# Kernel optimization log

Hardware: AMD Instinct MI355X
Metric: run time of the kernel (lower is better)

## Reference

```python
import jax, jax.numpy as jnp
import numpy as np

EMBED_DIM = 1024
NUM_HEADS = 16
HEAD_DIM = EMBED_DIM // NUM_HEADS


def setup_inputs() -> dict:
    key = jax.random.key(0)
    ks = jax.random.split(key, 9)
    B, S, E = 2, 2048, EMBED_DIM
    scale = 1.0 / np.sqrt(E)
    inp = {
        "x": jax.random.normal(ks[0], (B, S, E), dtype=jnp.float32),
        "Wq": jax.random.normal(ks[1], (E, E), dtype=jnp.float32) * scale,
        "bq": jnp.zeros((E,), dtype=jnp.float32),
        "Wk": jax.random.normal(ks[2], (E, E), dtype=jnp.float32) * scale,
        "bk": jnp.zeros((E,), dtype=jnp.float32),
        "Wv": jax.random.normal(ks[3], (E, E), dtype=jnp.float32) * scale,
        "bv": jnp.zeros((E,), dtype=jnp.float32),
        "Wo": jax.random.normal(ks[4], (E, E), dtype=jnp.float32) * scale,
        "bo": jnp.zeros((E,), dtype=jnp.float32),
    }
    return inp


def reference(x, Wq, bq, Wk, bk, Wv, bv, Wo, bo):
    B, S, E = x.shape
    H, D = NUM_HEADS, HEAD_DIM
    sm_scale = D ** (-0.5)

    def proj(W, b):
        # torch Linear: x @ W.T + b ; reshape to [B, H, S, D]
        y = jnp.einsum("bse,fe->bsf", x, W) + b
        return y.reshape(B, S, H, D).transpose(0, 2, 1, 3)

    q = proj(Wq, bq)  # [B, H, S, D]
    k = proj(Wk, bk)
    v = proj(Wv, bv)

    scores = jnp.einsum("bhqd,bhkd->bhqk", q, k) * sm_scale  # [B, H, S, S]
    attn = jax.nn.softmax(scores, axis=-1)
    o = jnp.einsum("bhqk,bhkd->bhqd", attn, v)  # [B, H, S, D]
    o = o.transpose(0, 2, 1, 3).reshape(B, S, E)
    return jnp.einsum("bse,fe->bsf", o, Wo) + bo
```

## Files before the change

kernel.cpp:

```cpp
#include <hip/hip_runtime.h>
#include <hip/hip_fp16.h>
#include <stdint.h>


typedef _Float16 f16;
typedef _Float16 f16x8 __attribute__((ext_vector_type(8)));
typedef _Float16 f16x4v __attribute__((ext_vector_type(4)));
typedef float f32x4 __attribute__((ext_vector_type(4)));
typedef int i32x4 __attribute__((ext_vector_type(4)));

#define BQ  2
#define SEQ 2048
#define EMB 1024
#define NH  16
#define HD  64
#define MM  (BQ * SEQ)

__device__ __forceinline__ void gld_lds16(const void* g, void* l) {
  __builtin_amdgcn_global_load_lds(
      (const __attribute__((address_space(1))) void*)g,
      (__attribute__((address_space(3))) void*)l, 16, 0, 0);
}

__device__ __forceinline__ void stage128x64(const f16* __restrict__ src,
                                            int ld, f16* lds, int tid) {
#pragma unroll
  for (int it = 0; it < 4; ++it) {
    int idx = it * 256 + tid;
    int r = idx >> 3, c = idx & 7;
    int sc = c ^ (r & 7);
    gld_lds16(src + (size_t)r * ld + sc * 8, lds + idx * 8);
  }
}

__device__ __forceinline__ f16x8 pack8(float a0, float a1, float a2, float a3,
                                       float b0, float b1, float b2, float b3) {
  i32x4 w;
  w.x = __builtin_bit_cast(int, __builtin_amdgcn_cvt_pkrtz(a0, a1));
  w.y = __builtin_bit_cast(int, __builtin_amdgcn_cvt_pkrtz(a2, a3));
  w.z = __builtin_bit_cast(int, __builtin_amdgcn_cvt_pkrtz(b0, b1));
  w.w = __builtin_bit_cast(int, __builtin_amdgcn_cvt_pkrtz(b2, b3));
  return __builtin_bit_cast(f16x8, w);
}

__global__ void cvtAll(const float* __restrict__ x, const float* __restrict__ w0,
                       const float* __restrict__ w1, const float* __restrict__ w2,
                       const float* __restrict__ w3, f16* __restrict__ dst) {
  int i = blockIdx.x * blockDim.x + threadIdx.x;
  const float* s;
  int off;
  if (i < (1 << 19)) {
    s = x; off = i;
  } else {
    int j = i - (1 << 19);
    int w = j >> 17, o = j & ((1 << 17) - 1);
    s = (w == 0) ? w0 : (w == 1) ? w1 : (w == 2) ? w2 : w3;
    off = o;
  }
  float4 v0 = ((const float4*)s)[2 * off];
  float4 v1 = ((const float4*)s)[2 * off + 1];
  ((f16x8*)dst)[i] = pack8(v0.x, v0.y, v0.z, v0.w, v1.x, v1.y, v1.z, v1.w);
}

template <int MODE>
__global__ __launch_bounds__(256, 2) void gemm_bt(
    const f16* __restrict__ A, const f16* __restrict__ W0,
    const f16* __restrict__ W1, const f16* __restrict__ W2,
    const float* __restrict__ b0, const float* __restrict__ b1,
    const float* __restrict__ b2, f16* __restrict__ o0, f16* __restrict__ o1,
    f16* __restrict__ o2, float* __restrict__ fo) {
  __shared__ __align__(16) f16 As[128 * 64];
  __shared__ __align__(16) f16 Bs[128 * 64];

  const int tid = threadIdx.x, lane = tid & 63, wid = tid >> 6;
  const int o = blockIdx.x;
  const int cx = o & 7, j = o >> 3;
  const int bx = 4 * cx + (j & 3);
  int by, z;
  if (MODE == 0) { int yz = j >> 2; by = yz & 7; z = yz >> 3; }
  else           { by = j >> 2; z = 0; }
  const f16* W = (z == 0) ? W0 : (z == 1 ? W1 : W2);
  const float* bia = (z == 0) ? b0 : (z == 1 ? b1 : b2);
  f16* outp = (z == 0) ? o0 : (z == 1 ? o1 : o2);
  const int row0 = bx * 128, col0 = by * 128;
  const bool vswap = (MODE == 0 && z == 2);
  const f16* Asrc = vswap ? W + (size_t)col0 * EMB : A + (size_t)row0 * EMB;
  const f16* Bsrc = vswap ? A + (size_t)row0 * EMB : W + (size_t)col0 * EMB;
  const int wr = (wid >> 1) * 64, wc = (wid & 1) * 64;
  const int rb = lane & 15, gq = lane >> 4, sw = lane & 7;

  f32x4 acc[4][4] = {};

  for (int kt = 0; kt < EMB / 64; ++kt) {
    __syncthreads();
    stage128x64(Asrc + kt * 64, EMB, As, tid);
    stage128x64(Bsrc + kt * 64, EMB, Bs, tid);
    asm volatile("s_waitcnt vmcnt(0)" ::: "memory");
    __syncthreads();
#pragma unroll
    for (int kk = 0; kk < 2; ++kk) {
      f16x8 av[4], bv[4];
#pragma unroll
      for (int f = 0; f < 4; ++f) {
        av[f] = *(const f16x8*)(As + (wr + f * 16 + rb) * 64 +
                                (((kk * 4 + gq) ^ sw) << 3));
        bv[f] = *(const f16x8*)(Bs + (wc + f * 16 + rb) * 64 +
                                (((kk * 4 + gq) ^ sw) << 3));
      }
#pragma unroll
      for (int fi = 0; fi < 4; ++fi)
#pragma unroll
        for (int fj = 0; fj < 4; ++fj)
          acc[fi][fj] = __builtin_amdgcn_mfma_f32_16x16x32_f16(
              av[fi], bv[fj], acc[fi][fj], 0, 0, 0);
    }
  }

  float bias[4];
  if (!vswap) {
#pragma unroll
    for (int fj = 0; fj < 4; ++fj) bias[fj] = bia[col0 + wc + fj * 16 + rb];
  }
  const float scale = (MODE == 0 && z == 0) ? 0.18033688011112042f : 1.0f;
#pragma unroll
  for (int fi = 0; fi < 4; ++fi) {
#pragma unroll
    for (int i = 0; i < 4; ++i) {
      const int lr = wr + fi * 16 + gq * 4 + i;
      const float brow = vswap ? bia[col0 + lr] : 0.f;
#pragma unroll
      for (int fj = 0; fj < 4; ++fj) {
        const int lc = wc + fj * 16 + rb;
        float v = acc[fi][fj][i] + (vswap ? brow : bias[fj]);
        v *= scale;
        if (MODE == 0) {
          if (vswap) {
            int e = col0 + lr, sg = row0 + lc;
            int h = e >> 6, d = e & 63;
            int b = sg >> 11, sl = sg & (SEQ - 1);
            int u = sl & 63;
            int p = ((u >> 5) << 5) + (((u >> 2) & 3) << 3) +
                    (((u >> 4) & 1) << 2) + (u & 3);
            int spos = (sl & ~63) | p;
            outp[((size_t)(b * NH + h) * HD + d) * SEQ + spos] = (f16)v;
          } else {
            int row = row0 + lr, col = col0 + lc;
            int bb = row >> 11, s = row & (SEQ - 1);
            int h = col >> 6, d = col & 63;
            outp[(((size_t)(bb * NH + h)) * SEQ + s) * HD + d] = (f16)v;
          }
        } else {
          fo[(size_t)(row0 + lr) * EMB + col0 + lc] = v;
        }
      }
    }
  }
}

__global__ __launch_bounds__(256, 2) void attn_fwd(const f16* __restrict__ Q,
                                                   const f16* __restrict__ K,
                                                   const f16* __restrict__ Vt,
                                                   f16* __restrict__ O) {
  __shared__ __align__(16) f16 Ks[2][2][64 * 64];
  __shared__ __align__(16) f16 Vs[2][2][64 * 64];

  const int tid = threadIdx.x, lane = tid & 63;
  const int wid = tid >> 6;
  const int orig = blockIdx.x;
  const int swz = ((orig & 7) << 6) + (orig >> 3);
  const int qt = swz & 15, bh = swz >> 4;
  const f16* Qh = Q + (size_t)bh * SEQ * HD;
  const f16* Kh = K + (size_t)bh * SEQ * HD;
  const f16* Vth = Vt + (size_t)bh * HD * SEQ;
  const int q0 = qt * 128 + wid * 32;
  const int rb = lane & 15, gq = lane >> 4, sw = lane & 7;

  f16x8 aq[2][2];
#pragma unroll
  for (int qf = 0; qf < 2; ++qf)
#pragma unroll
    for (int kk = 0; kk < 2; ++kk)
      aq[qf][kk] = *(const f16x8*)(Qh + (size_t)(q0 + qf * 16 + rb) * HD +
                                   kk * 32 + gq * 8);
  asm volatile("s_waitcnt vmcnt(0)" ::: "memory");

  const int srow = tid >> 3, scol = (tid & 7) ^ (srow & 7);
  const f16* Kg0 = Kh + (size_t)srow * HD + scol * 8;
  const f16* Vg0 = Vth + (size_t)srow * SEQ + scol * 8;

  const int NT2 = SEQ / 128;
#pragma unroll
  for (int sub = 0; sub < 2; ++sub) {
    const f16* kg = Kg0 + (size_t)sub * 64 * HD;
    const f16* vg = Vg0 + sub * 64;
    gld_lds16(kg,            &Ks[0][sub][tid * 8]);
    gld_lds16(kg + 32 * HD,  &Ks[0][sub][(tid + 256) * 8]);
    gld_lds16(vg,            &Vs[0][sub][tid * 8]);
    gld_lds16(vg + 32 * SEQ, &Vs[0][sub][(tid + 256) * 8]);
  }

  f16x8 ones;
#pragma unroll
  for (int j = 0; j < 8; ++j) ones[j] = (f16)1.0f;

  f32x4 oaccA[2][4] = {};
  f32x4 oaccB[2][4] = {};
  f32x4 lacc[2] = {};

  for (int t = 0; t < NT2; ++t) {
    __builtin_amdgcn_s_barrier();
    __builtin_amdgcn_sched_barrier(0);
    {
      const int tp = (t + 1 < NT2) ? t + 1 : NT2 - 1;
      const int ns = (t + 1) & 1;
#pragma unroll
      for (int sub = 0; sub < 2; ++sub) {
        const f16* kg = Kg0 + (size_t)(2 * tp + sub) * 64 * HD;
        const f16* vg = Vg0 + (2 * tp + sub) * 64;
        gld_lds16(kg,            &Ks[ns][sub][tid * 8]);
        gld_lds16(kg + 32 * HD,  &Ks[ns][sub][(tid + 256) * 8]);
        gld_lds16(vg,            &Vs[ns][sub][tid * 8]);
        gld_lds16(vg + 32 * SEQ, &Vs[ns][sub][(tid + 256) * 8]);
      }
      asm volatile("s_waitcnt vmcnt(8)" ::: "memory");
    }
    __builtin_amdgcn_s_barrier();
    __builtin_amdgcn_sched_barrier(0);

    const int cs = t & 1;
    const f16* Kb0 = &Ks[cs][0][0];
    const f16* Kb1 = &Ks[cs][1][0];
    const f16* Vb0 = &Vs[cs][0][0];
    const f16* Vb1 = &Vs[cs][1][0];

    __builtin_amdgcn_s_setprio(1);

    f32x4 s0_[2][4] = {};
#pragma unroll
    for (int kk = 0; kk < 2; ++kk) {
      f16x8 bk[4];
#pragma unroll
      for (int cf = 0; cf < 4; ++cf)
        bk[cf] = *(const f16x8*)(Kb0 + (cf * 16 + rb) * 64 +
                                 (((kk * 4 + gq) ^ sw) << 3));
#pragma unroll
      for (int qf = 0; qf < 2; ++qf)
#pragma unroll
        for (int cf = 0; cf < 4; ++cf)
          s0_[qf][cf] = __builtin_amdgcn_mfma_f32_16x16x32_f16(
              bk[cf], aq[qf][kk], s0_[qf][cf], 0, 0, 0);
    }

    f16x8 bp0[2][2];
#pragma unroll
    for (int qf = 0; qf < 2; ++qf)
#pragma unroll
      for (int g = 0; g < 2; ++g) {
        float e0 = __builtin_amdgcn_exp2f(s0_[qf][2 * g][0]);
        float e1 = __builtin_amdgcn_exp2f(s0_[qf][2 * g][1]);
        float e2 = __builtin_amdgcn_exp2f(s0_[qf][2 * g][2]);
        float e3 = __builtin_amdgcn_exp2f(s0_[qf][2 * g][3]);
        float f0 = __builtin_amdgcn_exp2f(s0_[qf][2 * g + 1][0]);
        float f1 = __builtin_amdgcn_exp2f(s0_[qf][2 * g + 1][1]);
        float f2 = __builtin_amdgcn_exp2f(s0_[qf][2 * g + 1][2]);
        float f3 = __builtin_amdgcn_exp2f(s0_[qf][2 * g + 1][3]);
        bp0[qf][g] = pack8(e0, e1, e2, e3, f0, f1, f2, f3);
      }

    f32x4 s1_[2][4] = {};
#pragma unroll
    for (int kk = 0; kk < 2; ++kk) {
      f16x8 bk[4];
#pragma unroll
      for (int cf = 0; cf < 4; ++cf)
        bk[cf] = *(const f16x8*)(Kb1 + (cf * 16 + rb) * 64 +
                                 (((kk * 4 + gq) ^ sw) << 3));
#pragma unroll
      for (int qf = 0; qf < 2; ++qf)
#pragma unroll
        for (int cf = 0; cf < 4; ++cf)
          s1_[qf][cf] = __builtin_amdgcn_mfma_f32_16x16x32_f16(
              bk[cf], aq[qf][kk], s1_[qf][cf], 0, 0, 0);
    }

#pragma unroll
    for (int g = 0; g < 2; ++g) {
      lacc[0] = __builtin_amdgcn_mfma_f32_16x16x32_f16(bp0[0][g], ones,
                                                       lacc[0], 0, 0, 0);
      lacc[1] = __builtin_amdgcn_mfma_f32_16x16x32_f16(bp0[1][g], ones,
                                                       lacc[1], 0, 0, 0);
#pragma unroll
      for (int df = 0; df < 4; ++df) {
        f16x8 vb = *(const f16x8*)(Vb0 + (df * 16 + rb) * 64 +
                                   (((g * 4 + gq) ^ sw) << 3));
        oaccA[0][df] = __builtin_amdgcn_mfma_f32_16x16x32_f16(
            bp0[0][g], vb, oaccA[0][df], 0, 0, 0);
        oaccA[1][df] = __builtin_amdgcn_mfma_f32_16x16x32_f16(
            bp0[1][g], vb, oaccA[1][df], 0, 0, 0);
      }
    }

    f16x8 bp1[2][2];
#pragma unroll
    for (int qf = 0; qf < 2; ++qf)
#pragma unroll
      for (int g = 0; g < 2; ++g) {
        float e0 = __builtin_amdgcn_exp2f(s1_[qf][2 * g][0]);
        float e1 = __builtin_amdgcn_exp2f(s1_[qf][2 * g][1]);
        float e2 = __builtin_amdgcn_exp2f(s1_[qf][2 * g][2]);
        float e3 = __builtin_amdgcn_exp2f(s1_[qf][2 * g][3]);
        float f0 = __builtin_amdgcn_exp2f(s1_[qf][2 * g + 1][0]);
        float f1 = __builtin_amdgcn_exp2f(s1_[qf][2 * g + 1][1]);
        float f2 = __builtin_amdgcn_exp2f(s1_[qf][2 * g + 1][2]);
        float f3 = __builtin_amdgcn_exp2f(s1_[qf][2 * g + 1][3]);
        bp1[qf][g] = pack8(e0, e1, e2, e3, f0, f1, f2, f3);
      }

#pragma unroll
    for (int g = 0; g < 2; ++g) {
      lacc[0] = __builtin_amdgcn_mfma_f32_16x16x32_f16(bp1[0][g], ones,
                                                       lacc[0], 0, 0, 0);
      lacc[1] = __builtin_amdgcn_mfma_f32_16x16x32_f16(bp1[1][g], ones,
                                                       lacc[1], 0, 0, 0);
#pragma unroll
      for (int df = 0; df < 4; ++df) {
        f16x8 vb = *(const f16x8*)(Vb1 + (df * 16 + rb) * 64 +
                                   (((g * 4 + gq) ^ sw) << 3));
        oaccB[0][df] = __builtin_amdgcn_mfma_f32_16x16x32_f16(
            bp1[0][g], vb, oaccB[0][df], 0, 0, 0);
        oaccB[1][df] = __builtin_amdgcn_mfma_f32_16x16x32_f16(
            bp1[1][g], vb, oaccB[1][df], 0, 0, 0);
      }
    }

    __builtin_amdgcn_s_setprio(0);
  }
  asm volatile("s_waitcnt vmcnt(0)" ::: "memory");

  const int b = bh >> 4, h = bh & 15;
#pragma unroll
  for (int qf = 0; qf < 2; ++qf)
#pragma unroll
    for (int i = 0; i < 4; ++i) {
      const float inv = 1.0f / lacc[qf][i];
      const int s = q0 + qf * 16 + gq * 4 + i;
      f16* orow = O + ((size_t)(b * SEQ + s)) * EMB + h * 64 + rb;
#pragma unroll
      for (int df = 0; df < 4; ++df)
        orow[df * 16] =
            (f16)((oaccA[qf][df][i] + oaccB[qf][df][i]) * inv);
    }
}

extern "C" void kernel_launch(void* const* d_in, const int* in_sizes, int n_in,
                              void* d_out, int out_size, void* d_ws,
                              size_t ws_size, hipStream_t stream) {
  const float* x = (const float*)d_in[0];
  const float* Wq = (const float*)d_in[1];
  const float* bq = (const float*)d_in[2];
  const float* Wk = (const float*)d_in[3];
  const float* bk = (const float*)d_in[4];
  const float* Wv = (const float*)d_in[5];
  const float* bv = (const float*)d_in[6];
  const float* Wo = (const float*)d_in[7];
  const float* bo = (const float*)d_in[8];
  float* out = (float*)d_out;

  const size_t NX = (size_t)MM * EMB;
  const size_t NW = (size_t)EMB * EMB;

  f16* xh  = (f16*)d_ws;
  f16* wqh = xh + NX;
  f16* wkh = wqh + NW;
  f16* wvh = wkh + NW;
  f16* woh = wvh + NW;
  f16* Qw  = woh + NW;
  f16* Kw  = Qw + NX;
  f16* Vtw = Kw + NX;
  f16* Ow  = Vtw + NX;

  cvtAll<<<dim3(4096), 256, 0, stream>>>(x, Wq, Wk, Wv, Wo, xh);

  gemm_bt<0><<<dim3(768), 256, 0, stream>>>(
      xh, wqh, wkh, wvh, bq, bk, bv, Qw, Kw, Vtw, nullptr);

  attn_fwd<<<dim3(512), 256, 0, stream>>>(Qw, Kw, Vtw, Ow);

  gemm_bt<1><<<dim3(256), 256, 0, stream>>>(
      Ow, woh, woh, woh, bo, bo, bo, nullptr, nullptr, nullptr, out);
}
```

Measured before the change: 101.7 us.

## Fuse fp32-to-fp16 conversion of x into the QKV projection GEMM

The QKV projection GEMM now loads fp32 x tiles straight into LDS with an XOR swizzle and converts them to fp16 while building MFMA fragments. This removes the separate conversion pass over x and the fp16 copy of it, so the conversion kernel only handles the weights. In exchange each block moves twice as many bytes for the A tile, uses more LDS (48KB), and repeats the conversion work across the 24 column blocks that share the same rows.

```diff
diff --git a/kernel.cpp b/kernel.cpp
--- a/kernel.cpp
+++ b/kernel.cpp
@@ -43,20 +43,21 @@
   return __builtin_bit_cast(f16x8, w);
 }
 
-__global__ void cvtAll(const float* __restrict__ x, const float* __restrict__ w0,
-                       const float* __restrict__ w1, const float* __restrict__ w2,
-                       const float* __restrict__ w3, f16* __restrict__ dst) {
+__device__ __forceinline__ f16x8 readXfrag(const float* Xs, int xr, int kk,
+                                           int gq) {
+  const int cb = kk * 8 + gq * 2;
+  const int m = xr & 15;
+  f32x4 a = *(const f32x4*)(Xs + xr * 64 + ((cb ^ m) << 2));
+  f32x4 b = *(const f32x4*)(Xs + xr * 64 + (((cb + 1) ^ m) << 2));
+  return pack8(a.x, a.y, a.z, a.w, b.x, b.y, b.z, b.w);
+}
+
+__global__ void cvtW(const float* __restrict__ w0, const float* __restrict__ w1,
+                     const float* __restrict__ w2, const float* __restrict__ w3,
+                     f16* __restrict__ dst) {
   int i = blockIdx.x * blockDim.x + threadIdx.x;
-  const float* s;
-  int off;
-  if (i < (1 << 19)) {
-    s = x; off = i;
-  } else {
-    int j = i - (1 << 19);
-    int w = j >> 17, o = j & ((1 << 17) - 1);
-    s = (w == 0) ? w0 : (w == 1) ? w1 : (w == 2) ? w2 : w3;
-    off = o;
-  }
+  int w = i >> 17, off = i & ((1 << 17) - 1);
+  const float* s = (w == 0) ? w0 : (w == 1) ? w1 : (w == 2) ? w2 : w3;
   float4 v0 = ((const float4*)s)[2 * off];
   float4 v1 = ((const float4*)s)[2 * off + 1];
   ((f16x8*)dst)[i] = pack8(v0.x, v0.y, v0.z, v0.w, v1.x, v1.y, v1.z, v1.w);
@@ -64,13 +65,14 @@
 
 template <int MODE>
 __global__ __launch_bounds__(256, 2) void gemm_bt(
-    const f16* __restrict__ A, const f16* __restrict__ W0,
+    const void* __restrict__ Aaw, const f16* __restrict__ W0,
     const f16* __restrict__ W1, const f16* __restrict__ W2,
     const float* __restrict__ b0, const float* __restrict__ b1,
     const float* __restrict__ b2, f16* __restrict__ o0, f16* __restrict__ o1,
     f16* __restrict__ o2, float* __restrict__ fo) {
-  __shared__ __align__(16) f16 As[128 * 64];
-  __shared__ __align__(16) f16 Bs[128 * 64];
+  constexpr int SMEMB =
+      (MODE == 0) ? (128 * 64 * 4 + 128 * 64 * 2) : (2 * 128 * 64 * 2);
+  __shared__ __align__(16) unsigned char smem[SMEMB];
 
   const int tid = threadIdx.x, lane = tid & 63, wid = tid >> 6;
   const int o = blockIdx.x;
@@ -84,35 +86,82 @@
   f16* outp = (z == 0) ? o0 : (z == 1 ? o1 : o2);
   const int row0 = bx * 128, col0 = by * 128;
   const bool vswap = (MODE == 0 && z == 2);
-  const f16* Asrc = vswap ? W + (size_t)col0 * EMB : A + (size_t)row0 * EMB;
-  const f16* Bsrc = vswap ? A + (size_t)row0 * EMB : W + (size_t)col0 * EMB;
   const int wr = (wid >> 1) * 64, wc = (wid & 1) * 64;
   const int rb = lane & 15, gq = lane >> 4, sw = lane & 7;
 
   f32x4 acc[4][4] = {};
 
-  for (int kt = 0; kt < EMB / 64; ++kt) {
-    __syncthreads();
-    stage128x64(Asrc + kt * 64, EMB, As, tid);
-    stage128x64(Bsrc + kt * 64, EMB, Bs, tid);
-    asm volatile("s_waitcnt vmcnt(0)" ::: "memory");
-    __syncthreads();
-#pragma unroll
-    for (int kk = 0; kk < 2; ++kk) {
-      f16x8 av[4], bv[4];
-#pragma unroll
-      for (int f = 0; f < 4; ++f) {
-        av[f] = *(const f16x8*)(As + (wr + f * 16 + rb) * 64 +
-                                (((kk * 4 + gq) ^ sw) << 3));
-        bv[f] = *(const f16x8*)(Bs + (wc + f * 16 + rb) * 64 +
-                                (((kk * 4 + gq) ^ sw) << 3));
-      }
-#pragma unroll
-      for (int fi = 0; fi < 4; ++fi)
-#pragma unroll
-        for (int fj = 0; fj < 4; ++fj)
-          acc[fi][fj] = __builtin_amdgcn_mfma_f32_16x16x32_f16(
-              av[fi], bv[fj], acc[fi][fj], 0, 0, 0);
+  if constexpr (MODE == 0) {
+    const float* xf = (const float*)Aaw;
+    float* Xs = (float*)smem;
+    f16* Ws = (f16*)(smem + 128 * 64 * 4);
+
+    for (int kt = 0; kt < EMB / 64; ++kt) {
+      __syncthreads();
+      stage128x64(W + (size_t)col0 * EMB + kt * 64, EMB, Ws, tid);
+#pragma unroll
+      for (int it = 0; it < 8; ++it) {
+        int idx = it * 256 + tid;
+        int r = idx >> 4, c = idx & 15;
+        int sc = c ^ (r & 15);
+        gld_lds16(xf + (size_t)(row0 + r) * EMB + kt * 64 + sc * 4,
+                  (unsigned char*)Xs + idx * 16);
+      }
+      asm volatile("s_waitcnt vmcnt(0)" ::: "memory");
+      __syncthreads();
+#pragma unroll
+      for (int kk = 0; kk < 2; ++kk) {
+        f16x8 av[4], bv[4];
+        if (!vswap) {
+#pragma unroll
+          for (int f = 0; f < 4; ++f) {
+            av[f] = readXfrag(Xs, wr + f * 16 + rb, kk, gq);
+            bv[f] = *(const f16x8*)(Ws + (wc + f * 16 + rb) * 64 +
+                                    (((kk * 4 + gq) ^ sw) << 3));
+          }
+        } else {
+#pragma unroll
+          for (int f = 0; f < 4; ++f) {
+            av[f] = *(const f16x8*)(Ws + (wr + f * 16 + rb) * 64 +
+                                    (((kk * 4 + gq) ^ sw) << 3));
+            bv[f] = readXfrag(Xs, wc + f * 16 + rb, kk, gq);
+          }
+        }
+#pragma unroll
+        for (int fi = 0; fi < 4; ++fi)
+#pragma unroll
+          for (int fj = 0; fj < 4; ++fj)
+            acc[fi][fj] = __builtin_amdgcn_mfma_f32_16x16x32_f16(
+                av[fi], bv[fj], acc[fi][fj], 0, 0, 0);
+      }
+    }
+  } else {
+    const f16* ah = (const f16*)Aaw;
+    f16* As = (f16*)smem;
+    f16* Bs = (f16*)(smem + 128 * 64 * 2);
+    for (int kt = 0; kt < EMB / 64; ++kt) {
+      __syncthreads();
+      stage128x64(ah + (size_t)row0 * EMB + kt * 64, EMB, As, tid);
+      stage128x64(W + (size_t)col0 * EMB + kt * 64, EMB, Bs, tid);
+      asm volatile("s_waitcnt vmcnt(0)" ::: "memory");
+      __syncthreads();
+#pragma unroll
+      for (int kk = 0; kk < 2; ++kk) {
+        f16x8 av[4], bv[4];
+#pragma unroll
+        for (int f = 0; f < 4; ++f) {
+          av[f] = *(const f16x8*)(As + (wr + f * 16 + rb) * 64 +
+                                  (((kk * 4 + gq) ^ sw) << 3));
+          bv[f] = *(const f16x8*)(Bs + (wc + f * 16 + rb) * 64 +
+                                  (((kk * 4 + gq) ^ sw) << 3));
+        }
+#pragma unroll
+        for (int fi = 0; fi < 4; ++fi)
+#pragma unroll
+          for (int fj = 0; fj < 4; ++fj)
+            acc[fi][fj] = __builtin_amdgcn_mfma_f32_16x16x32_f16(
+                av[fi], bv[fj], acc[fi][fj], 0, 0, 0);
+      }
     }
   }
 
@@ -369,8 +418,7 @@
   const size_t NX = (size_t)MM * EMB;
   const size_t NW = (size_t)EMB * EMB;
 
-  f16* xh  = (f16*)d_ws;
-  f16* wqh = xh + NX;
+  f16* wqh = (f16*)d_ws;
   f16* wkh = wqh + NW;
   f16* wvh = wkh + NW;
   f16* woh = wvh + NW;
@@ -379,10 +427,10 @@
   f16* Vtw = Kw + NX;
   f16* Ow  = Vtw + NX;
 
-  cvtAll<<<dim3(4096), 256, 0, stream>>>(x, Wq, Wk, Wv, Wo, xh);
+  cvtW<<<dim3(2048), 256, 0, stream>>>(Wq, Wk, Wv, Wo, wqh);
 
   gemm_bt<0><<<dim3(768), 256, 0, stream>>>(
-      xh, wqh, wkh, wvh, bq, bk, bv, Qw, Kw, Vtw, nullptr);
+      x, wqh, wkh, wvh, bq, bk, bv, Qw, Kw, Vtw, nullptr);
 
   attn_fwd<<<dim3(512), 256, 0, stream>>>(Qw, Kw, Vtw, Ow);
 
```

Result: slower. 109.1 us (+7.3%).

## Read K and V tiles directly from global memory instead of LDS staging

Applied to the files above, without the earlier changes.

Removes the double-buffered LDS staging of K and V (async global-to-LDS loads, barriers, swizzle, setprio) from the attention kernel, and has each wave load its MFMA operands straight from global memory through the cache. This drops the barrier synchronisation and LDS traffic, but every wave now fetches the same K/V data separately. It also loses the prefetch overlap, so each iteration waits on global-load latency.

```diff
diff --git a/kernel.cpp b/kernel.cpp
--- a/kernel.cpp
+++ b/kernel.cpp
@@ -161,9 +161,6 @@
                                                    const f16* __restrict__ K,
                                                    const f16* __restrict__ Vt,
                                                    f16* __restrict__ O) {
-  __shared__ __align__(16) f16 Ks[2][2][64 * 64];
-  __shared__ __align__(16) f16 Vs[2][2][64 * 64];
-
   const int tid = threadIdx.x, lane = tid & 63;
   const int wid = tid >> 6;
   const int orig = blockIdx.x;
@@ -173,7 +170,7 @@
   const f16* Kh = K + (size_t)bh * SEQ * HD;
   const f16* Vth = Vt + (size_t)bh * HD * SEQ;
   const int q0 = qt * 128 + wid * 32;
-  const int rb = lane & 15, gq = lane >> 4, sw = lane & 7;
+  const int rb = lane & 15, gq = lane >> 4;
 
   f16x8 aq[2][2];
 #pragma unroll
@@ -182,22 +179,6 @@
     for (int kk = 0; kk < 2; ++kk)
       aq[qf][kk] = *(const f16x8*)(Qh + (size_t)(q0 + qf * 16 + rb) * HD +
                                    kk * 32 + gq * 8);
-  asm volatile("s_waitcnt vmcnt(0)" ::: "memory");
-
-  const int srow = tid >> 3, scol = (tid & 7) ^ (srow & 7);
-  const f16* Kg0 = Kh + (size_t)srow * HD + scol * 8;
-  const f16* Vg0 = Vth + (size_t)srow * SEQ + scol * 8;
-
-  const int NT2 = SEQ / 128;
-#pragma unroll
-  for (int sub = 0; sub < 2; ++sub) {
-    const f16* kg = Kg0 + (size_t)sub * 64 * HD;
-    const f16* vg = Vg0 + sub * 64;
-    gld_lds16(kg,            &Ks[0][sub][tid * 8]);
-    gld_lds16(kg + 32 * HD,  &Ks[0][sub][(tid + 256) * 8]);
-    gld_lds16(vg,            &Vs[0][sub][tid * 8]);
-    gld_lds16(vg + 32 * SEQ, &Vs[0][sub][(tid + 256) * 8]);
-  }
 
   f16x8 ones;
 #pragma unroll
@@ -207,33 +188,13 @@
   f32x4 oaccB[2][4] = {};
   f32x4 lacc[2] = {};
 
+  const int NT2 = SEQ / 128;
   for (int t = 0; t < NT2; ++t) {
-    __builtin_amdgcn_s_barrier();
-    __builtin_amdgcn_sched_barrier(0);
-    {
-      const int tp = (t + 1 < NT2) ? t + 1 : NT2 - 1;
-      const int ns = (t + 1) & 1;
-#pragma unroll
-      for (int sub = 0; sub < 2; ++sub) {
-        const f16* kg = Kg0 + (size_t)(2 * tp + sub) * 64 * HD;
-        const f16* vg = Vg0 + (2 * tp + sub) * 64;
-        gld_lds16(kg,            &Ks[ns][sub][tid * 8]);
-        gld_lds16(kg + 32 * HD,  &Ks[ns][sub][(tid + 256) * 8]);
-        gld_lds16(vg,            &Vs[ns][sub][tid * 8]);
-        gld_lds16(vg + 32 * SEQ, &Vs[ns][sub][(tid + 256) * 8]);
-      }
-      asm volatile("s_waitcnt vmcnt(8)" ::: "memory");
-    }
-    __builtin_amdgcn_s_barrier();
-    __builtin_amdgcn_sched_barrier(0);
-
-    const int cs = t & 1;
-    const f16* Kb0 = &Ks[cs][0][0];
-    const f16* Kb1 = &Ks[cs][1][0];
-    const f16* Vb0 = &Vs[cs][0][0];
-    const f16* Vb1 = &Vs[cs][1][0];
-
-    __builtin_amdgcn_s_setprio(1);
+    const int kv0 = t * 128;
+    const f16* Kb0 = Kh + (size_t)kv0 * HD;
+    const f16* Kb1 = Kb0 + 64 * HD;
+    const f16* Vb0 = Vth + kv0;
+    const f16* Vb1 = Vb0 + 64;
 
     f32x4 s0_[2][4] = {};
 #pragma unroll
@@ -241,8 +202,8 @@
       f16x8 bk[4];
 #pragma unroll
       for (int cf = 0; cf < 4; ++cf)
-        bk[cf] = *(const f16x8*)(Kb0 + (cf * 16 + rb) * 64 +
-                                 (((kk * 4 + gq) ^ sw) << 3));
+        bk[cf] = *(const f16x8*)(Kb0 + (size_t)(cf * 16 + rb) * HD +
+                                 (kk * 4 + gq) * 8);
 #pragma unroll
       for (int qf = 0; qf < 2; ++qf)
 #pragma unroll
@@ -273,8 +234,8 @@
       f16x8 bk[4];
 #pragma unroll
       for (int cf = 0; cf < 4; ++cf)
-        bk[cf] = *(const f16x8*)(Kb1 + (cf * 16 + rb) * 64 +
-                                 (((kk * 4 + gq) ^ sw) << 3));
+        bk[cf] = *(const f16x8*)(Kb1 + (size_t)(cf * 16 + rb) * HD +
+                                 (kk * 4 + gq) * 8);
 #pragma unroll
       for (int qf = 0; qf < 2; ++qf)
 #pragma unroll
@@ -291,8 +252,8 @@
                                                        lacc[1], 0, 0, 0);
 #pragma unroll
       for (int df = 0; df < 4; ++df) {
-        f16x8 vb = *(const f16x8*)(Vb0 + (df * 16 + rb) * 64 +
-                                   (((g * 4 + gq) ^ sw) << 3));
+        f16x8 vb = *(const f16x8*)(Vb0 + (size_t)(df * 16 + rb) * SEQ +
+                                   (4 * g + gq) * 8);
         oaccA[0][df] = __builtin_amdgcn_mfma_f32_16x16x32_f16(
             bp0[0][g], vb, oaccA[0][df], 0, 0, 0);
         oaccA[1][df] = __builtin_amdgcn_mfma_f32_16x16x32_f16(
@@ -324,18 +285,15 @@
                                                        lacc[1], 0, 0, 0);
 #pragma unroll
       for (int df = 0; df < 4; ++df) {
-        f16x8 vb = *(const f16x8*)(Vb1 + (df * 16 + rb) * 64 +
-                                   (((g * 4 + gq) ^ sw) << 3));
+        f16x8 vb = *(const f16x8*)(Vb1 + (size_t)(df * 16 + rb) * SEQ +
+                                   (4 * g + gq) * 8);
         oaccB[0][df] = __builtin_amdgcn_mfma_f32_16x16x32_f16(
             bp1[0][g], vb, oaccB[0][df], 0, 0, 0);
         oaccB[1][df] = __builtin_amdgcn_mfma_f32_16x16x32_f16(
             bp1[1][g], vb, oaccB[1][df], 0, 0, 0);
       }
     }
-
-    __builtin_amdgcn_s_setprio(0);
-  }
-  asm volatile("s_waitcnt vmcnt(0)" ::: "memory");
+  }
 
   const int b = bh >> 4, h = bh & 15;
 #pragma unroll
```

Measured after the change: 178.3 us. 1.75x slower.
